# Kernel tuning notes

Measured on AMD Instinct MI355X. Metric: run time of the kernel, lower is better.

## Reference

```python
import jax, jax.numpy as jnp
import numpy as np

B, T, D, H = 2, 2048, 512, 8
HD = D // H  # head_dim = 64


def setup_inputs() -> dict:
    key = jax.random.key(0)
    k1, k2, k3, k4 = jax.random.split(key, 4)
    scale = 1.0 / np.sqrt(D)
    x = jax.random.normal(k1, (B, T, D), dtype=jnp.float32)
    periods = jax.random.randint(k2, (B, H), 0, 64, dtype=jnp.int32)
    w_qkv = jax.random.normal(k3, (3 * D, D), dtype=jnp.float32) * scale
    b_qkv = jnp.zeros((3 * D,), dtype=jnp.float32)
    w_out = jax.random.normal(k4, (D, D), dtype=jnp.float32) * scale
    b_out = jnp.zeros((D,), dtype=jnp.float32)
    return {"x": x, "periods": periods, "w_qkv": w_qkv, "b_qkv": b_qkv,
            "w_out": w_out, "b_out": b_out}


def reference(x, periods, w_qkv, b_qkv, w_out, b_out):
    # qkv projection: (B,T,3D) -> (3,B,H,T,HD)
    qkv = x @ w_qkv.T + b_qkv
    qkv = qkv.reshape(B, T, 3, H, HD).transpose(2, 0, 3, 1, 4)
    q, k, v = qkv[0], qkv[1], qkv[2]

    # periodic-causal mask: valid iff j <= i and (i-j) % p == 0, p = max(period,1)
    i_idx = jnp.arange(T, dtype=jnp.int32)[:, None]   # (T,1)
    j_idx = jnp.arange(T, dtype=jnp.int32)[None, :]   # (1,T)
    diff = i_idx - j_idx                              # (T,T)
    p = jnp.maximum(periods, 1)[:, :, None, None]     # (B,H,1,1)
    valid = (diff >= 0) & ((diff % p) == 0)           # (B,H,T,T)

    scores = jnp.einsum('bhqd,bhkd->bhqk', q, k) / np.sqrt(HD)
    scores = jnp.where(valid, scores, jnp.finfo(scores.dtype).min)
    attn = jax.nn.softmax(scores, axis=-1)

    out = jnp.einsum('bhqk,bhkd->bhqd', attn, v)
    out = out.transpose(0, 2, 1, 3).reshape(B, T, D)
    return out @ w_out.T + b_out
```

## Files before the change

kernel.cpp:

```cpp
#include <hip/hip_runtime.h>
#include <math.h>

#define B_  2
#define T_  2048
#define D_  512
#define H_  8
#define HD_ 64
#define QKVS (3*D_)

typedef __bf16 bf16x8 __attribute__((ext_vector_type(8)));
typedef float  f32x4  __attribute__((ext_vector_type(4)));

__device__ inline unsigned short f2bf(float f) {
  unsigned int u = __float_as_uint(f);
  return (unsigned short)((u + 0x7FFFu + ((u >> 16) & 1u)) >> 16);
}
__device__ inline unsigned int pack2bf(float lo, float hi) {
  return (unsigned int)f2bf(lo) | ((unsigned int)f2bf(hi) << 16);
}

__global__ void cast_all(const float* __restrict__ x,
                         const float* __restrict__ wq,
                         const float* __restrict__ wo,
                         unsigned short* __restrict__ xb,
                         unsigned short* __restrict__ wqb,
                         unsigned short* __restrict__ wob) {
  const int n_x  = (B_ * T_ * D_) / 4;
  const int n_wq = (QKVS * D_) / 4;
  const int n_wo = (D_ * D_) / 4;
  int i = blockIdx.x * blockDim.x + threadIdx.x;
  const float* src; unsigned short* dst; int off;
  if (i < n_x)                    { src = x;  dst = xb;  off = i; }
  else if (i < n_x + n_wq)        { src = wq; dst = wqb; off = i - n_x; }
  else if (i < n_x + n_wq + n_wo) { src = wo; dst = wob; off = i - n_x - n_wq; }
  else return;
  float4 v = ((const float4*)src)[off];
  ushort4 o;
  o.x = f2bf(v.x); o.y = f2bf(v.y); o.z = f2bf(v.z); o.w = f2bf(v.w);
  ((ushort4*)dst)[off] = o;
}

template<int BF16OUT>
__global__ __launch_bounds__(256)
void gemm_nt_mfma(const unsigned short* __restrict__ A,
                  const unsigned short* __restrict__ Bw,
                  const float* __restrict__ bias, void* __restrict__ Cv,
                  int M, int N, int K) {
  __shared__ short Asd[128 * 32];
  __shared__ short Bsd[64 * 32];

  const int tid = threadIdx.x;
  const int w   = tid >> 6;
  const int l   = tid & 63;
  const int wr  = w >> 1;
  const int wc  = w & 1;
  const int q   = l >> 4;
  const int ml  = l & 15;
  const int arow = l >> 2;
  const int kch  = (l & 3) * 8;

  const int rowbase = blockIdx.y * 128;
  const int colbase = blockIdx.x * 64;

  f32x4 acc[4][2] = {};

  for (int k0 = 0; k0 < K; k0 += 32) {
    __syncthreads();
    #pragma unroll
    for (int s = 0; s < 2; ++s) {
      const unsigned short* g =
          A + (size_t)(rowbase + s * 64 + w * 16 + arow) * K + k0 + kch;
      __builtin_amdgcn_global_load_lds(
          (const __attribute__((address_space(1))) void*)g,
          (__attribute__((address_space(3))) void*)&Asd[s * 2048 + w * 512],
          16, 0, 0);
    }
    {
      const unsigned short* g =
          Bw + (size_t)(colbase + w * 16 + arow) * K + k0 + kch;
      __builtin_amdgcn_global_load_lds(
          (const __attribute__((address_space(1))) void*)g,
          (__attribute__((address_space(3))) void*)&Bsd[w * 512], 16, 0, 0);
    }
    __syncthreads();

    bf16x8 af[4], bfr[2];
    #pragma unroll
    for (int mi = 0; mi < 4; ++mi)
      af[mi] = *(const bf16x8*)&Asd[(wr * 64 + mi * 16 + ml) * 32 + q * 8];
    #pragma unroll
    for (int ni = 0; ni < 2; ++ni)
      bfr[ni] = *(const bf16x8*)&Bsd[(wc * 32 + ni * 16 + ml) * 32 + q * 8];
    #pragma unroll
    for (int mi = 0; mi < 4; ++mi)
      #pragma unroll
      for (int ni = 0; ni < 2; ++ni)
        acc[mi][ni] = __builtin_amdgcn_mfma_f32_16x16x32_bf16(
            af[mi], bfr[ni], acc[mi][ni], 0, 0, 0);
  }

  #pragma unroll
  for (int mi = 0; mi < 4; ++mi) {
    #pragma unroll
    for (int ni = 0; ni < 2; ++ni) {
      const int col = colbase + wc * 32 + ni * 16 + ml;
      const float bv = bias[col];
      #pragma unroll
      for (int r = 0; r < 4; ++r) {
        const int row = rowbase + wr * 64 + mi * 16 + q * 4 + r;
        const float val = acc[mi][ni][r] + bv;
        if (BF16OUT)
          ((unsigned short*)Cv)[(size_t)row * N + col] = f2bf(val);
        else
          ((float*)Cv)[(size_t)row * N + col] = val;
      }
    }
  }
}

template<int BF16OUT>
__global__ __launch_bounds__(256)
void gemm_nt_mfma128(const unsigned short* __restrict__ A,
                     const unsigned short* __restrict__ Bw,
                     const float* __restrict__ bias, void* __restrict__ Cv,
                     int M, int N, int K) {
  __shared__ short Asd[128 * 32];
  __shared__ short Bsd[128 * 32];

  const int tid = threadIdx.x;
  const int w   = tid >> 6;
  const int l   = tid & 63;
  const int wr  = w >> 1;
  const int wc  = w & 1;
  const int q   = l >> 4;
  const int ml  = l & 15;
  const int arow = l >> 2;
  const int kch  = (l & 3) * 8;

  const int rowbase = blockIdx.y * 128;
  const int colbase = blockIdx.x * 128;

  f32x4 acc[4][4] = {};

  for (int k0 = 0; k0 < K; k0 += 32) {
    __syncthreads();
    #pragma unroll
    for (int s = 0; s < 2; ++s) {
      const unsigned short* ga =
          A + (size_t)(rowbase + s * 64 + w * 16 + arow) * K + k0 + kch;
      __builtin_amdgcn_global_load_lds(
          (const __attribute__((address_space(1))) void*)ga,
          (__attribute__((address_space(3))) void*)&Asd[s * 2048 + w * 512],
          16, 0, 0);
      const unsigned short* gb =
          Bw + (size_t)(colbase + s * 64 + w * 16 + arow) * K + k0 + kch;
      __builtin_amdgcn_global_load_lds(
          (const __attribute__((address_space(1))) void*)gb,
          (__attribute__((address_space(3))) void*)&Bsd[s * 2048 + w * 512],
          16, 0, 0);
    }
    __syncthreads();

    bf16x8 af[4], bfr[4];
    #pragma unroll
    for (int mi = 0; mi < 4; ++mi)
      af[mi] = *(const bf16x8*)&Asd[(wr * 64 + mi * 16 + ml) * 32 + q * 8];
    #pragma unroll
    for (int ni = 0; ni < 4; ++ni)
      bfr[ni] = *(const bf16x8*)&Bsd[(wc * 64 + ni * 16 + ml) * 32 + q * 8];
    #pragma unroll
    for (int mi = 0; mi < 4; ++mi)
      #pragma unroll
      for (int ni = 0; ni < 4; ++ni)
        acc[mi][ni] = __builtin_amdgcn_mfma_f32_16x16x32_bf16(
            af[mi], bfr[ni], acc[mi][ni], 0, 0, 0);
  }

  #pragma unroll
  for (int mi = 0; mi < 4; ++mi) {
    #pragma unroll
    for (int ni = 0; ni < 4; ++ni) {
      const int col = colbase + wc * 64 + ni * 16 + ml;
      const float bv = bias[col];
      #pragma unroll
      for (int r = 0; r < 4; ++r) {
        const int row = rowbase + wr * 64 + mi * 16 + q * 4 + r;
        const float val = acc[mi][ni][r] + bv;
        if (BF16OUT)
          ((unsigned short*)Cv)[(size_t)row * N + col] = f2bf(val);
        else
          ((float*)Cv)[(size_t)row * N + col] = val;
      }
    }
  }
}

__global__ __launch_bounds__(256)
void attn_flash2(const unsigned short* __restrict__ qkv,
                 const int* __restrict__ periods,
                 unsigned short* __restrict__ ao) {
  const int bh = blockIdx.x, slot = 62 - blockIdx.y;
  int p = periods[bh]; if (p < 1) p = 1;
  const int g  = slot / p;
  const int r  = slot - g * p;
  const int L  = (T_ - 1 - r) / p + 1;
  const int q0 = g << 6;
  if (q0 >= L) return;
  const int b = bh >> 3, h = bh & 7;
  const int Lrem = L - q0;
  const int Nkb  = min(L, q0 + 64);

  const int tid  = threadIdx.x;
  const int w    = tid >> 6;
  const int lane = tid & 63;
  const int Q = lane >> 4, c = lane & 15;

  __shared__ __align__(16) unsigned short Qs[64 * 72];
  __shared__ __align__(16) unsigned short Ks[32 * 72];
  __shared__ __align__(16) unsigned short Vt[64 * 40];

  const size_t rowb = (size_t)b * T_ * QKVS + (size_t)h * HD_;

  {
    const int u = tid >> 2, ch4 = (tid & 3) * 16;
    const int t = q0 + min(u, Lrem - 1);
    const unsigned short* gq = qkv + rowb + (size_t)(r + t * p) * QKVS + ch4;
    int4 v0 = ((const int4*)gq)[0];
    int4 v1 = ((const int4*)gq)[1];
    *(int4*)&Qs[u * 72 + ch4 + 0] = v0;
    *(int4*)&Qs[u * 72 + ch4 + 8] = v1;
  }
  __syncthreads();
  bf16x8 qf[2];
  qf[0] = *(const bf16x8*)&Qs[(w * 16 + c) * 72 + Q * 8];
  qf[1] = *(const bf16x8*)&Qs[(w * 16 + c) * 72 + Q * 8 + 32];

  const int qb      = w * 16;
  const int nqw     = min(16, Lrem - qb);
  const int qglob   = q0 + qb + c;
  const int mylastk = q0 + qb + 15;

  float m_run = -3.0e38f, l_run = 0.f;
  f32x4 o[4] = {};
  const size_t kb = rowb + D_;
  const size_t vb = rowb + 2 * D_;

  const int krow = tid >> 3, koff = (tid & 7) * 8;
  const int vkey = tid & 31, vd0 = (tid >> 5) * 8;

  int4 kvp, vvp;
  {
    const int tk = min(krow, Nkb - 1);
    const int tv = min(vkey, Nkb - 1);
    kvp = *(const int4*)(qkv + kb + (size_t)(r + tk * p) * QKVS + koff);
    vvp = *(const int4*)(qkv + vb + (size_t)(r + tv * p) * QKVS + vd0);
  }

  for (int k0 = 0; k0 < Nkb; k0 += 32) {
    __syncthreads();
    {
      unsigned short vh[8];
      *(int4*)vh = vvp;
      *(int4*)&Ks[krow * 72 + koff] = kvp;
      #pragma unroll
      for (int j = 0; j < 8; ++j)
        Vt[(vd0 + j) * 40 + vkey] = vh[j];
    }
    __syncthreads();

    if (k0 + 32 < Nkb) {
      const int tk = min(k0 + 32 + krow, Nkb - 1);
      const int tv = min(k0 + 32 + vkey, Nkb - 1);
      kvp = *(const int4*)(qkv + kb + (size_t)(r + tk * p) * QKVS + koff);
      vvp = *(const int4*)(qkv + vb + (size_t)(r + tv * p) * QKVS + vd0);
    }

    if (nqw > 0 && k0 <= mylastk) {
      f32x4 s[2];
      #pragma unroll
      for (int mt = 0; mt < 2; ++mt) {
        bf16x8 a0 = *(const bf16x8*)&Ks[(mt * 16 + c) * 72 + Q * 8];
        bf16x8 a1 = *(const bf16x8*)&Ks[(mt * 16 + c) * 72 + Q * 8 + 32];
        f32x4 acc = {};
        acc = __builtin_amdgcn_mfma_f32_16x16x32_bf16(a0, qf[0], acc, 0, 0, 0);
        acc = __builtin_amdgcn_mfma_f32_16x16x32_bf16(a1, qf[1], acc, 0, 0, 0);
        s[mt] = acc;
      }

      float pvv[8];
      float tmax = -3.0e38f;
      #pragma unroll
      for (int mt = 0; mt < 2; ++mt)
        #pragma unroll
        for (int rg = 0; rg < 4; ++rg) {
          const int kk = k0 + mt * 16 + Q * 4 + rg;
          float v = s[mt][rg] * 0.125f;
          v = (kk <= qglob) ? v : -3.0e38f;
          pvv[mt * 4 + rg] = v;
          tmax = fmaxf(tmax, v);
        }
      tmax = fmaxf(tmax, __shfl_xor(tmax, 16));
      tmax = fmaxf(tmax, __shfl_xor(tmax, 32));
      const float m_new = fmaxf(m_run, tmax);
      const float alpha = __expf(m_run - m_new);
      float tsum = 0.f;
      #pragma unroll
      for (int i = 0; i < 8; ++i) { pvv[i] = __expf(pvv[i] - m_new); tsum += pvv[i]; }
      tsum += __shfl_xor(tsum, 16);
      tsum += __shfl_xor(tsum, 32);
      l_run = l_run * alpha + tsum;
      m_run = m_new;

      unsigned int pk0[2], pk1[2];
      pk0[0] = pack2bf(pvv[0], pvv[1]); pk0[1] = pack2bf(pvv[2], pvv[3]);
      pk1[0] = pack2bf(pvv[4], pvv[5]); pk1[1] = pack2bf(pvv[6], pvv[7]);
      int dw[4];
      const int sq2 = (Q & 1) << 1;
      #pragma unroll
      for (int d = 0; d < 4; ++d) {
        const int src = ((sq2 + (d >> 1)) << 4) + c;
        const int v0 = __shfl((int)pk0[d & 1], src);
        const int v1 = __shfl((int)pk1[d & 1], src);
        dw[d] = (Q >= 2) ? v1 : v0;
      }
      int4 bi = make_int4(dw[0], dw[1], dw[2], dw[3]);
      bf16x8 pb = *(bf16x8*)&bi;

      #pragma unroll
      for (int ch = 0; ch < 4; ++ch) {
        bf16x8 af = *(const bf16x8*)&Vt[(ch * 16 + c) * 40 + Q * 8];
        f32x4 oo = o[ch];
        #pragma unroll
        for (int t2 = 0; t2 < 4; ++t2) oo[t2] *= alpha;
        o[ch] = __builtin_amdgcn_mfma_f32_16x16x32_bf16(af, pb, oo, 0, 0, 0);
      }
    }
  }

  if (nqw > 0 && c < nqw) {
    const float invl = 1.f / l_run;
    const int tok = r + (q0 + qb + c) * p;
    unsigned int* dst =
        (unsigned int*)(ao + (size_t)(b * T_ + tok) * D_ + h * HD_);
    #pragma unroll
    for (int ch = 0; ch < 4; ++ch)
      #pragma unroll
      for (int rp = 0; rp < 2; ++rp) {
        const int dhalf = ch * 16 + Q * 4 + rp * 2;
        dst[dhalf >> 1] =
            pack2bf(o[ch][rp * 2] * invl, o[ch][rp * 2 + 1] * invl);
      }
  }
}

extern "C" void kernel_launch(void* const* d_in, const int* in_sizes, int n_in,
                              void* d_out, int out_size, void* d_ws, size_t ws_size,
                              hipStream_t stream) {
  const float* x      = (const float*)d_in[0];
  const int*   period = (const int*)  d_in[1];
  const float* w_qkv  = (const float*)d_in[2];
  const float* b_qkv  = (const float*)d_in[3];
  const float* w_out  = (const float*)d_in[4];
  const float* b_out  = (const float*)d_in[5];
  float* out = (float*)d_out;

  const int M = B_ * T_;

  char* ws = (char*)d_ws;
  unsigned short* xb   = (unsigned short*)(ws);
  unsigned short* wqb  = (unsigned short*)(ws + (size_t)M * D_ * 2);
  unsigned short* wob  = (unsigned short*)(ws + (size_t)M * D_ * 2
                                              + (size_t)QKVS * D_ * 2);
  unsigned short* qkvb = (unsigned short*)(ws + (size_t)M * D_ * 2
                                              + (size_t)QKVS * D_ * 2
                                              + (size_t)D_ * D_ * 2);
  unsigned short* aob  = xb;

  {
    const int n4 = (M * D_ + QKVS * D_ + D_ * D_) / 4;
    cast_all<<<dim3((n4 + 255) / 256), dim3(256), 0, stream>>>(
        x, w_qkv, w_out, xb, wqb, wob);
  }

  gemm_nt_mfma128<1><<<dim3(QKVS / 128, M / 128), dim3(256), 0, stream>>>(
      xb, wqb, b_qkv, qkvb, M, QKVS, D_);

  attn_flash2<<<dim3(16, 63), dim3(256), 0, stream>>>(qkvb, period, aob);

  gemm_nt_mfma<0><<<dim3(D_ / 64, M / 128), dim3(256), 0, stream>>>(
      aob, wob, b_out, out, M, D_, D_);
}
```

Measured before the change: 113.4 us.

## Widen attention key tile to 64 and use BK=64 GEMM for both projections

The attention kernel now stages 64 keys per iteration instead of 32, which halves the barrier and online-softmax rescale steps. It skips QK and PV MFMAs for 16/32-key sub-tiles beyond the wave's last valid key. Both GEMMs now use a single 128x64 kernel that loads two K=32 panels per barrier (BK=64), with launch bounds set for 3 blocks per SIMD. The QKV projection drops its 128x128 tile for this smaller-N tile, giving more blocks but less reuse per block. Attention also needs more LDS.

```diff
diff --git a/kernel.cpp b/kernel.cpp
--- a/kernel.cpp
+++ b/kernel.cpp
@@ -41,13 +41,13 @@
 }
 
 template<int BF16OUT>
-__global__ __launch_bounds__(256)
-void gemm_nt_mfma(const unsigned short* __restrict__ A,
+__global__ __launch_bounds__(256, 3)
+void gemm_nt_bk64(const unsigned short* __restrict__ A,
                   const unsigned short* __restrict__ Bw,
                   const float* __restrict__ bias, void* __restrict__ Cv,
                   int M, int N, int K) {
-  __shared__ short Asd[128 * 32];
-  __shared__ short Bsd[64 * 32];
+  __shared__ short Asd[2][128 * 32];
+  __shared__ short Bsd[2][64 * 32];
 
   const int tid = threadIdx.x;
   const int w   = tid >> 6;
@@ -64,39 +64,45 @@
 
   f32x4 acc[4][2] = {};
 
-  for (int k0 = 0; k0 < K; k0 += 32) {
+  for (int k0 = 0; k0 < K; k0 += 64) {
     __syncthreads();
     #pragma unroll
-    for (int s = 0; s < 2; ++s) {
+    for (int pnl = 0; pnl < 2; ++pnl) {
+      const int kp = k0 + pnl * 32;
+      #pragma unroll
+      for (int s = 0; s < 2; ++s) {
+        const unsigned short* g =
+            A + (size_t)(rowbase + s * 64 + w * 16 + arow) * K + kp + kch;
+        __builtin_amdgcn_global_load_lds(
+            (const __attribute__((address_space(1))) void*)g,
+            (__attribute__((address_space(3))) void*)
+                &Asd[pnl][s * 2048 + w * 512], 16, 0, 0);
+      }
       const unsigned short* g =
-          A + (size_t)(rowbase + s * 64 + w * 16 + arow) * K + k0 + kch;
+          Bw + (size_t)(colbase + w * 16 + arow) * K + kp + kch;
       __builtin_amdgcn_global_load_lds(
           (const __attribute__((address_space(1))) void*)g,
-          (__attribute__((address_space(3))) void*)&Asd[s * 2048 + w * 512],
+          (__attribute__((address_space(3))) void*)&Bsd[pnl][w * 512],
           16, 0, 0);
     }
-    {
-      const unsigned short* g =
-          Bw + (size_t)(colbase + w * 16 + arow) * K + k0 + kch;
-      __builtin_amdgcn_global_load_lds(
-          (const __attribute__((address_space(1))) void*)g,
-          (__attribute__((address_space(3))) void*)&Bsd[w * 512], 16, 0, 0);
-    }
     __syncthreads();
 
-    bf16x8 af[4], bfr[2];
     #pragma unroll
-    for (int mi = 0; mi < 4; ++mi)
-      af[mi] = *(const bf16x8*)&Asd[(wr * 64 + mi * 16 + ml) * 32 + q * 8];
-    #pragma unroll
-    for (int ni = 0; ni < 2; ++ni)
-      bfr[ni] = *(const bf16x8*)&Bsd[(wc * 32 + ni * 16 + ml) * 32 + q * 8];
-    #pragma unroll
-    for (int mi = 0; mi < 4; ++mi)
+    for (int pnl = 0; pnl < 2; ++pnl) {
+      bf16x8 af[4], bfr[2];
+      #pragma unroll
+      for (int mi = 0; mi < 4; ++mi)
+        af[mi] = *(const bf16x8*)&Asd[pnl][(wr * 64 + mi * 16 + ml) * 32 + q * 8];
       #pragma unroll
       for (int ni = 0; ni < 2; ++ni)
-        acc[mi][ni] = __builtin_amdgcn_mfma_f32_16x16x32_bf16(
-            af[mi], bfr[ni], acc[mi][ni], 0, 0, 0);
+        bfr[ni] = *(const bf16x8*)&Bsd[pnl][(wc * 32 + ni * 16 + ml) * 32 + q * 8];
+      #pragma unroll
+      for (int mi = 0; mi < 4; ++mi)
+        #pragma unroll
+        for (int ni = 0; ni < 2; ++ni)
+          acc[mi][ni] = __builtin_amdgcn_mfma_f32_16x16x32_bf16(
+              af[mi], bfr[ni], acc[mi][ni], 0, 0, 0);
+    }
   }
 
   #pragma unroll
@@ -118,85 +124,8 @@
   }
 }
 
-template<int BF16OUT>
 __global__ __launch_bounds__(256)
-void gemm_nt_mfma128(const unsigned short* __restrict__ A,
-                     const unsigned short* __restrict__ Bw,
-                     const float* __restrict__ bias, void* __restrict__ Cv,
-                     int M, int N, int K) {
-  __shared__ short Asd[128 * 32];
-  __shared__ short Bsd[128 * 32];
-
-  const int tid = threadIdx.x;
-  const int w   = tid >> 6;
-  const int l   = tid & 63;
-  const int wr  = w >> 1;
-  const int wc  = w & 1;
-  const int q   = l >> 4;
-  const int ml  = l & 15;
-  const int arow = l >> 2;
-  const int kch  = (l & 3) * 8;
-
-  const int rowbase = blockIdx.y * 128;
-  const int colbase = blockIdx.x * 128;
-
-  f32x4 acc[4][4] = {};
-
-  for (int k0 = 0; k0 < K; k0 += 32) {
-    __syncthreads();
-    #pragma unroll
-    for (int s = 0; s < 2; ++s) {
-      const unsigned short* ga =
-          A + (size_t)(rowbase + s * 64 + w * 16 + arow) * K + k0 + kch;
-      __builtin_amdgcn_global_load_lds(
-          (const __attribute__((address_space(1))) void*)ga,
-          (__attribute__((address_space(3))) void*)&Asd[s * 2048 + w * 512],
-          16, 0, 0);
-      const unsigned short* gb =
-          Bw + (size_t)(colbase + s * 64 + w * 16 + arow) * K + k0 + kch;
-      __builtin_amdgcn_global_load_lds(
-          (const __attribute__((address_space(1))) void*)gb,
-          (__attribute__((address_space(3))) void*)&Bsd[s * 2048 + w * 512],
-          16, 0, 0);
-    }
-    __syncthreads();
-
-    bf16x8 af[4], bfr[4];
-    #pragma unroll
-    for (int mi = 0; mi < 4; ++mi)
-      af[mi] = *(const bf16x8*)&Asd[(wr * 64 + mi * 16 + ml) * 32 + q * 8];
-    #pragma unroll
-    for (int ni = 0; ni < 4; ++ni)
-      bfr[ni] = *(const bf16x8*)&Bsd[(wc * 64 + ni * 16 + ml) * 32 + q * 8];
-    #pragma unroll
-    for (int mi = 0; mi < 4; ++mi)
-      #pragma unroll
-      for (int ni = 0; ni < 4; ++ni)
-        acc[mi][ni] = __builtin_amdgcn_mfma_f32_16x16x32_bf16(
-            af[mi], bfr[ni], acc[mi][ni], 0, 0, 0);
-  }
-
-  #pragma unroll
-  for (int mi = 0; mi < 4; ++mi) {
-    #pragma unroll
-    for (int ni = 0; ni < 4; ++ni) {
-      const int col = colbase + wc * 64 + ni * 16 + ml;
-      const float bv = bias[col];
-      #pragma unroll
-      for (int r = 0; r < 4; ++r) {
-        const int row = rowbase + wr * 64 + mi * 16 + q * 4 + r;
-        const float val = acc[mi][ni][r] + bv;
-        if (BF16OUT)
-          ((unsigned short*)Cv)[(size_t)row * N + col] = f2bf(val);
-        else
-          ((float*)Cv)[(size_t)row * N + col] = val;
-      }
-    }
-  }
-}
-
-__global__ __launch_bounds__(256)
-void attn_flash2(const unsigned short* __restrict__ qkv,
+void attn_flash4(const unsigned short* __restrict__ qkv,
                  const int* __restrict__ periods,
                  unsigned short* __restrict__ ao) {
   const int bh = blockIdx.x, slot = 62 - blockIdx.y;
@@ -216,8 +145,8 @@
   const int Q = lane >> 4, c = lane & 15;
 
   __shared__ __align__(16) unsigned short Qs[64 * 72];
-  __shared__ __align__(16) unsigned short Ks[32 * 72];
-  __shared__ __align__(16) unsigned short Vt[64 * 40];
+  __shared__ __align__(16) unsigned short Ks[64 * 72];
+  __shared__ __align__(16) unsigned short Vt[64 * 72];
 
   const size_t rowb = (size_t)b * T_ * QKVS + (size_t)h * HD_;
 
@@ -245,94 +174,124 @@
   const size_t kb = rowb + D_;
   const size_t vb = rowb + 2 * D_;
 
-  const int krow = tid >> 3, koff = (tid & 7) * 8;
-  const int vkey = tid & 31, vd0 = (tid >> 5) * 8;
-
-  int4 kvp, vvp;
+  const int krow = tid >> 2, koff = (tid & 3) * 16;
+  const int vkey = tid & 63, vd0 = (tid >> 6) * 8;
+
+  int4 kp0, kp1, vp0, vp1;
   {
     const int tk = min(krow, Nkb - 1);
     const int tv = min(vkey, Nkb - 1);
-    kvp = *(const int4*)(qkv + kb + (size_t)(r + tk * p) * QKVS + koff);
-    vvp = *(const int4*)(qkv + vb + (size_t)(r + tv * p) * QKVS + vd0);
-  }
-
-  for (int k0 = 0; k0 < Nkb; k0 += 32) {
+    const unsigned short* gk = qkv + kb + (size_t)(r + tk * p) * QKVS + koff;
+    const unsigned short* gv = qkv + vb + (size_t)(r + tv * p) * QKVS;
+    kp0 = ((const int4*)gk)[0];
+    kp1 = ((const int4*)gk)[1];
+    vp0 = *(const int4*)(gv + vd0);
+    vp1 = *(const int4*)(gv + vd0 + 32);
+  }
+
+  for (int k0 = 0; k0 < Nkb; k0 += 64) {
     __syncthreads();
     {
-      unsigned short vh[8];
-      *(int4*)vh = vvp;
-      *(int4*)&Ks[krow * 72 + koff] = kvp;
-      #pragma unroll
-      for (int j = 0; j < 8; ++j)
-        Vt[(vd0 + j) * 40 + vkey] = vh[j];
+      *(int4*)&Ks[krow * 72 + koff + 0] = kp0;
+      *(int4*)&Ks[krow * 72 + koff + 8] = kp1;
+      unsigned short vh0[8], vh1[8];
+      *(int4*)vh0 = vp0;
+      *(int4*)vh1 = vp1;
+      #pragma unroll
+      for (int j = 0; j < 8; ++j) {
+        Vt[(vd0 + j) * 72 + vkey]      = vh0[j];
+        Vt[(vd0 + 32 + j) * 72 + vkey] = vh1[j];
+      }
     }
     __syncthreads();
 
-    if (k0 + 32 < Nkb) {
-      const int tk = min(k0 + 32 + krow, Nkb - 1);
-      const int tv = min(k0 + 32 + vkey, Nkb - 1);
-      kvp = *(const int4*)(qkv + kb + (size_t)(r + tk * p) * QKVS + koff);
-      vvp = *(const int4*)(qkv + vb + (size_t)(r + tv * p) * QKVS + vd0);
+    if (k0 + 64 < Nkb) {
+      const int tk = min(k0 + 64 + krow, Nkb - 1);
+      const int tv = min(k0 + 64 + vkey, Nkb - 1);
+      const unsigned short* gk = qkv + kb + (size_t)(r + tk * p) * QKVS + koff;
+      const unsigned short* gv = qkv + vb + (size_t)(r + tv * p) * QKVS;
+      kp0 = ((const int4*)gk)[0];
+      kp1 = ((const int4*)gk)[1];
+      vp0 = *(const int4*)(gv + vd0);
+      vp1 = *(const int4*)(gv + vd0 + 32);
     }
 
     if (nqw > 0 && k0 <= mylastk) {
-      f32x4 s[2];
-      #pragma unroll
-      for (int mt = 0; mt < 2; ++mt) {
-        bf16x8 a0 = *(const bf16x8*)&Ks[(mt * 16 + c) * 72 + Q * 8];
-        bf16x8 a1 = *(const bf16x8*)&Ks[(mt * 16 + c) * 72 + Q * 8 + 32];
-        f32x4 acc = {};
-        acc = __builtin_amdgcn_mfma_f32_16x16x32_bf16(a0, qf[0], acc, 0, 0, 0);
-        acc = __builtin_amdgcn_mfma_f32_16x16x32_bf16(a1, qf[1], acc, 0, 0, 0);
-        s[mt] = acc;
-      }
-
-      float pvv[8];
+      float pvv[16];
       float tmax = -3.0e38f;
       #pragma unroll
-      for (int mt = 0; mt < 2; ++mt)
-        #pragma unroll
-        for (int rg = 0; rg < 4; ++rg) {
-          const int kk = k0 + mt * 16 + Q * 4 + rg;
-          float v = s[mt][rg] * 0.125f;
-          v = (kk <= qglob) ? v : -3.0e38f;
-          pvv[mt * 4 + rg] = v;
-          tmax = fmaxf(tmax, v);
+      for (int mt = 0; mt < 4; ++mt) {
+        if (k0 + mt * 16 <= mylastk) {
+          bf16x8 a0 = *(const bf16x8*)&Ks[(mt * 16 + c) * 72 + Q * 8];
+          bf16x8 a1 = *(const bf16x8*)&Ks[(mt * 16 + c) * 72 + Q * 8 + 32];
+          f32x4 s = {};
+          s = __builtin_amdgcn_mfma_f32_16x16x32_bf16(a0, qf[0], s, 0, 0, 0);
+          s = __builtin_amdgcn_mfma_f32_16x16x32_bf16(a1, qf[1], s, 0, 0, 0);
+          #pragma unroll
+          for (int rg = 0; rg < 4; ++rg) {
+            const int kk = k0 + mt * 16 + Q * 4 + rg;
+            float v = s[rg] * 0.125f;
+            v = (kk <= qglob) ? v : -3.0e38f;
+            pvv[mt * 4 + rg] = v;
+            tmax = fmaxf(tmax, v);
+          }
+        } else {
+          #pragma unroll
+          for (int rg = 0; rg < 4; ++rg) pvv[mt * 4 + rg] = -3.0e38f;
         }
+      }
+
       tmax = fmaxf(tmax, __shfl_xor(tmax, 16));
       tmax = fmaxf(tmax, __shfl_xor(tmax, 32));
       const float m_new = fmaxf(m_run, tmax);
       const float alpha = __expf(m_run - m_new);
       float tsum = 0.f;
       #pragma unroll
-      for (int i = 0; i < 8; ++i) { pvv[i] = __expf(pvv[i] - m_new); tsum += pvv[i]; }
+      for (int i = 0; i < 16; ++i) {
+        pvv[i] = __expf(pvv[i] - m_new);
+        tsum += pvv[i];
+      }
       tsum += __shfl_xor(tsum, 16);
       tsum += __shfl_xor(tsum, 32);
       l_run = l_run * alpha + tsum;
       m_run = m_new;
 
-      unsigned int pk0[2], pk1[2];
-      pk0[0] = pack2bf(pvv[0], pvv[1]); pk0[1] = pack2bf(pvv[2], pvv[3]);
-      pk1[0] = pack2bf(pvv[4], pvv[5]); pk1[1] = pack2bf(pvv[6], pvv[7]);
-      int dw[4];
+      bf16x8 pb[2];
       const int sq2 = (Q & 1) << 1;
       #pragma unroll
-      for (int d = 0; d < 4; ++d) {
-        const int src = ((sq2 + (d >> 1)) << 4) + c;
-        const int v0 = __shfl((int)pk0[d & 1], src);
-        const int v1 = __shfl((int)pk1[d & 1], src);
-        dw[d] = (Q >= 2) ? v1 : v0;
-      }
-      int4 bi = make_int4(dw[0], dw[1], dw[2], dw[3]);
-      bf16x8 pb = *(bf16x8*)&bi;
-
-      #pragma unroll
-      for (int ch = 0; ch < 4; ++ch) {
-        bf16x8 af = *(const bf16x8*)&Vt[(ch * 16 + c) * 40 + Q * 8];
-        f32x4 oo = o[ch];
+      for (int kc = 0; kc < 2; ++kc) {
+        unsigned int pk0[2], pk1[2];
+        pk0[0] = pack2bf(pvv[kc * 8 + 0], pvv[kc * 8 + 1]);
+        pk0[1] = pack2bf(pvv[kc * 8 + 2], pvv[kc * 8 + 3]);
+        pk1[0] = pack2bf(pvv[kc * 8 + 4], pvv[kc * 8 + 5]);
+        pk1[1] = pack2bf(pvv[kc * 8 + 6], pvv[kc * 8 + 7]);
+        int dw[4];
         #pragma unroll
-        for (int t2 = 0; t2 < 4; ++t2) oo[t2] *= alpha;
-        o[ch] = __builtin_amdgcn_mfma_f32_16x16x32_bf16(af, pb, oo, 0, 0, 0);
+        for (int d = 0; d < 4; ++d) {
+          const int src = ((sq2 + (d >> 1)) << 4) + c;
+          const int v0 = __shfl((int)pk0[d & 1], src);
+          const int v1 = __shfl((int)pk1[d & 1], src);
+          dw[d] = (Q >= 2) ? v1 : v0;
+        }
+        int4 bi = make_int4(dw[0], dw[1], dw[2], dw[3]);
+        pb[kc] = *(bf16x8*)&bi;
+      }
+
+      #pragma unroll
+      for (int ch = 0; ch < 4; ++ch)
+        #pragma unroll
+        for (int t2 = 0; t2 < 4; ++t2) o[ch][t2] *= alpha;
+      #pragma unroll
+      for (int kc = 0; kc < 2; ++kc) {
+        if (k0 + kc * 32 <= mylastk) {
+          #pragma unroll
+          for (int ch = 0; ch < 4; ++ch) {
+            bf16x8 af =
+                *(const bf16x8*)&Vt[(ch * 16 + c) * 72 + kc * 32 + Q * 8];
+            o[ch] = __builtin_amdgcn_mfma_f32_16x16x32_bf16(af, pb[kc], o[ch],
+                                                            0, 0, 0);
+          }
+        }
       }
     }
   }
@@ -382,11 +341,11 @@
         x, w_qkv, w_out, xb, wqb, wob);
   }
 
-  gemm_nt_mfma128<1><<<dim3(QKVS / 128, M / 128), dim3(256), 0, stream>>>(
+  gemm_nt_bk64<1><<<dim3(QKVS / 64, M / 128), dim3(256), 0, stream>>>(
       xb, wqb, b_qkv, qkvb, M, QKVS, D_);
 
-  attn_flash2<<<dim3(16, 63), dim3(256), 0, stream>>>(qkvb, period, aob);
-
-  gemm_nt_mfma<0><<<dim3(D_ / 64, M / 128), dim3(256), 0, stream>>>(
+  attn_flash4<<<dim3(16, 63), dim3(256), 0, stream>>>(qkvb, period, aob);
+
+  gemm_nt_bk64<0><<<dim3(D_ / 64, M / 128), dim3(256), 0, stream>>>(
       aob, wob, b_out, out, M, D_, D_);
 }
```

After: 107.9 us. -4.9%, faster.
